# Kernel tuning notes

Measured on AMD Instinct MI355X. Metric: run time of the kernel, lower is better.

## Reference

```python
import jax, jax.numpy as jnp
import numpy as np

SIGMA = 4.0
KSIZE = 2 * int(4.0 * SIGMA + 0.5) + 1  # 33, anomalib AnomalyMapGenerator default


def _gauss_kernel():
    x = jnp.arange(KSIZE, dtype=jnp.float32) - (KSIZE - 1) / 2.0
    g = jnp.exp(-0.5 * (x / SIGMA) ** 2)
    return g / g.sum()


def _blur(img):
    # img: (B,1,H,W); separable Gaussian with reflect padding (kornia border_type='reflect')
    k = _gauss_kernel()
    p = (KSIZE - 1) // 2
    dn = ('NCHW', 'OIHW', 'NCHW')
    x = jnp.pad(img, ((0, 0), (0, 0), (p, p), (0, 0)), mode='reflect')
    x = jax.lax.conv_general_dilated(x, k.reshape(1, 1, KSIZE, 1), (1, 1), 'VALID', dimension_numbers=dn)
    x = jnp.pad(x, ((0, 0), (0, 0), (0, 0), (p, p)), mode='reflect')
    return jax.lax.conv_general_dilated(x, k.reshape(1, 1, 1, KSIZE), (1, 1), 'VALID', dimension_numbers=dn)


def _edist(x, y):
    # ||x-y||_2 via expanded quadratic, clamped at 0 (matches torch euclidean_dist)
    x2 = jnp.sum(x * x, axis=-1, keepdims=True)
    y2 = jnp.sum(y * y, axis=-1, keepdims=True)
    d2 = x2 - 2.0 * (x @ y.T) + y2.T
    return jnp.sqrt(jnp.clip(d2, 0.0))


def setup_inputs() -> dict:
    key = jax.random.key(0)
    k1, k2 = jax.random.split(key)
    return {
        'embedding': jax.random.normal(k1, (6272, 128), dtype=jnp.float32),
        'memory_bank': jax.random.normal(k2, (32768, 128), dtype=jnp.float32),
        'batch_size': 8,
        'width': 28,
        'height': 28,
        'out_size': 224,
        'num_neighbors': 9,
    }


def reference(embedding, memory_bank, batch_size, width, height, out_size, num_neighbors):
    N, D = embedding.shape
    M = memory_bank.shape[0]
    # --- nearest_neighbors(embedding, n_neighbors=1), euclidean metric ---
    dist = _edist(embedding, memory_bank)            # (N, M) dominant intermediate
    patch_scores = jnp.min(dist, axis=1)             # (N,)
    locations = jnp.argmin(dist, axis=1)             # (N,)
    P = N // batch_size
    patch_scores = patch_scores.reshape(batch_size, P)
    locations = locations.reshape(batch_size, P)
    # --- compute_anomaly_score (num_neighbors > 1 branch) ---
    b_idx = jnp.arange(batch_size)
    max_p = jnp.argmax(patch_scores, axis=1)                         # (B,)
    max_feat = embedding.reshape(batch_size, P, D)[b_idx, max_p]     # (B, D)
    score = patch_scores[b_idx, max_p]                               # (B,)
    nn_idx = locations[b_idx, max_p]                                 # (B,)
    nn_sample = memory_bank[nn_idx]                                  # (B, D)
    k = min(int(num_neighbors), M)
    d_nn = _edist(nn_sample, memory_bank)                            # (B, M)
    _, support = jax.lax.top_k(-d_nn, k)                             # (B, k) smallest distances
    mem_s = memory_bank[support]                                     # (B, k, D)
    qm = jnp.einsum('bd,bkd->bk', max_feat, mem_s)
    d2 = jnp.sum(max_feat * max_feat, -1, keepdims=True) - 2.0 * qm + jnp.sum(mem_s * mem_s, -1)
    dists = jnp.sqrt(jnp.clip(d2, 0.0))                              # (B, k)
    weights = (1.0 - jax.nn.softmax(dists, axis=1))[:, 0]
    pred_score = weights * score                                     # (B,)
    # --- anomaly map: bilinear upsample (align_corners=False) + Gaussian blur ---
    pm = patch_scores.reshape(batch_size, 1, width, height)
    amap = jax.image.resize(pm, (batch_size, 1, out_size, out_size), method='bilinear')
    anomaly_map = _blur(amap)
    return pred_score, anomaly_map
```

## Files before the change

### kernel.cpp

```cpp
#include <hip/hip_runtime.h>
#include <hip/hip_bf16.h>

#define N_EMB   6272
#define M_BANK  32768
#define D_DIM   128
#define KPA     128
#define KPB     128
#define BATCH   8
#define P_PATCH 784
#define GRID_WH 28
#define OUT_WH  224
#define KNN     9
#define KSIZE   33
#define KRAD    16

typedef unsigned long long ull;
typedef short bf16x8 __attribute__((ext_vector_type(8)));
typedef float f32x4  __attribute__((ext_vector_type(4)));

#define WS_MINPACK 0
#define WS_X2      50176
#define WS_Y2      75264
#define WS_BSCORE  231424
#define WS_BMAXP   231456
#define WS_BNN     231488
#define WS_DNN     231552
#define WS_APK     2885888
#define WS_BPK     7702784
#define WS_CAND    32868608

__device__ __forceinline__ ull umin64(ull a, ull b) { return a < b ? a : b; }
__device__ __forceinline__ ull umax64(ull a, ull b) { return a > b ? a : b; }

__device__ __forceinline__ void gload_lds16(const void* g, void* l) {
    __builtin_amdgcn_global_load_lds(
        (const __attribute__((address_space(1))) void*)g,
        (__attribute__((address_space(3))) void*)l, 16, 0, 0);
}

__global__ __launch_bounds__(256) void prep_kernel(
    const float* __restrict__ emb, const float* __restrict__ bank,
    unsigned short* __restrict__ Apk, unsigned short* __restrict__ Bpk,
    float* __restrict__ x2, float* __restrict__ y2, ull* __restrict__ minpack)
{
    const int tid = threadIdx.x;
    int gi = blockIdx.x * 256 + tid;
    if (gi < N_EMB) minpack[gi] = ~0ull;

    const int w    = blockIdx.x * 4 + (tid >> 6);
    const int lane = tid & 63;

    const float* src;
    unsigned short* dst;
    float* sq;
    if (w < N_EMB) {
        src = emb + (size_t)w * D_DIM;
        dst = Apk + (size_t)w * KPA;
        sq  = x2 + w;
    } else {
        int m = w - N_EMB;
        src = bank + (size_t)m * D_DIM;
        dst = Bpk + (size_t)m * KPB;
        sq  = y2 + m;
    }
    float2 v = *(const float2*)&src[2 * lane];
    __hip_bfloat16 h0 = __float2bfloat16(v.x);
    __hip_bfloat16 h1 = __float2bfloat16(v.y);
    unsigned hb0 = *(unsigned short*)&h0, hb1 = *(unsigned short*)&h1;
    *(unsigned*)&dst[2 * lane] = hb0 | (hb1 << 16);

    float s = fmaf(v.x, v.x, v.y * v.y);
    #pragma unroll
    for (int off = 32; off > 0; off >>= 1) s += __shfl_down(s, off, 64);
    if (lane == 0) *sq = s;
}

__global__ __launch_bounds__(256, 4) void mfma_min_kernel(
    const unsigned short* __restrict__ Apk, const unsigned short* __restrict__ Bpk,
    const float* __restrict__ y2, ull* __restrict__ minpack)
{
    __shared__ __align__(16) unsigned short smem[4 * 128 * 32];
    const int PAN = 128 * 32;

    const int tid  = threadIdx.x;
    const int lane = tid & 63;
    const int wave = tid >> 6;
    const int wr = wave >> 1, wc = wave & 1;
    const int n0 = blockIdx.y * 128;
    const int m0 = blockIdx.x * 128;

    const int srow = tid >> 2;
    const int sseg = tid & 3;
    const int ssw  = sseg ^ ((srow >> 1) & 3);

    const int qa = lane >> 4;
    const int ra = lane & 15;
    const int qsw = qa ^ ((ra >> 1) & 3);

    f32x4 acc[4][4];
    #pragma unroll
    for (int i = 0; i < 4; ++i)
        #pragma unroll
        for (int j = 0; j < 4; ++j)
            acc[i][j] = (f32x4){0.f, 0.f, 0.f, 0.f};

    const unsigned short* gA = Apk + (size_t)(n0 + srow) * KPA + ssw * 8;
    const unsigned short* gB = Bpk + (size_t)(m0 + srow) * KPB + ssw * 8;
    const int lof0 = srow * 32 + sseg * 8;
    const int lof1 = (srow + 64) * 32 + sseg * 8;

    gload_lds16(gA,            &smem[lof0]);
    gload_lds16(gA + 64 * KPA, &smem[lof1]);
    gload_lds16(gB,            &smem[2 * PAN + lof0]);
    gload_lds16(gB + 64 * KPB, &smem[2 * PAN + lof1]);

    #define STEP(s, VM) { \
         \
        asm volatile("s_barrier" ::: "memory"); \
        if ((s) < 3) { \
            const int ko = ((s) + 1) * 32; \
            const int nb = ((s) + 1) & 1; \
            gload_lds16(gA + ko,            &smem[nb * PAN + lof0]); \
            gload_lds16(gA + ko + 64 * KPA, &smem[nb * PAN + lof1]); \
            gload_lds16(gB + ko,            &smem[(2 + nb) * PAN + lof0]); \
            gload_lds16(gB + ko + 64 * KPB, &smem[(2 + nb) * PAN + lof1]); \
        } \
         \
        asm volatile("s_waitcnt vmcnt(" #VM ")" ::: "memory"); \
         \
        asm volatile("s_barrier" ::: "memory"); \
        const unsigned short* As = &smem[((s) & 1) * PAN]; \
        const unsigned short* Bs = &smem[(2 + ((s) & 1)) * PAN]; \
        bf16x8 bfr[4]; \
        _Pragma("unroll") \
        for (int j = 0; j < 4; ++j) \
            bfr[j] = *(const bf16x8*)&Bs[(wc * 64 + j * 16 + ra) * 32 + qsw * 8]; \
        { \
            bf16x8 af0 = *(const bf16x8*)&As[(wr * 64 +  0 + ra) * 32 + qsw * 8]; \
            bf16x8 af1 = *(const bf16x8*)&As[(wr * 64 + 16 + ra) * 32 + qsw * 8]; \
            _Pragma("unroll") \
            for (int j = 0; j < 4; ++j) \
                acc[0][j] = __builtin_amdgcn_mfma_f32_16x16x32_bf16(af0, bfr[j], acc[0][j], 0, 0, 0); \
            _Pragma("unroll") \
            for (int j = 0; j < 4; ++j) \
                acc[1][j] = __builtin_amdgcn_mfma_f32_16x16x32_bf16(af1, bfr[j], acc[1][j], 0, 0, 0); \
            __builtin_amdgcn_sched_barrier(0); \
            bf16x8 af2 = *(const bf16x8*)&As[(wr * 64 + 32 + ra) * 32 + qsw * 8]; \
            bf16x8 af3 = *(const bf16x8*)&As[(wr * 64 + 48 + ra) * 32 + qsw * 8]; \
            _Pragma("unroll") \
            for (int j = 0; j < 4; ++j) \
                acc[2][j] = __builtin_amdgcn_mfma_f32_16x16x32_bf16(af2, bfr[j], acc[2][j], 0, 0, 0); \
            _Pragma("unroll") \
            for (int j = 0; j < 4; ++j) \
                acc[3][j] = __builtin_amdgcn_mfma_f32_16x16x32_bf16(af3, bfr[j], acc[3][j], 0, 0, 0); \
        } \
    }

    STEP(0, 4) STEP(1, 4) STEP(2, 4) STEP(3, 0)
    #undef STEP

    float y2k[4];
    unsigned mj[4];
    #pragma unroll
    for (int j = 0; j < 4; ++j) {
        const int m = m0 + wc * 64 + j * 16 + ra;
        y2k[j] = y2[m] + 1000.0f;
        mj[j]  = (unsigned)m;
    }

    ull (*red2)[32] = (ull (*)[32])smem;

    __syncthreads();

    #pragma unroll
    for (int i = 0; i < 4; ++i) {
        #pragma unroll
        for (int r = 0; r < 4; ++r) {
            const int rowl = wr * 64 + i * 16 + qa * 4 + r;
            ull mn = ~0ull;
            #pragma unroll
            for (int j = 0; j < 4; ++j) {
                float key = fmaf(-2.0f, acc[i][j][r], y2k[j]);
                ull p = ((ull)__float_as_uint(key) << 32) | mj[j];
                mn = umin64(mn, p);
            }
            red2[rowl][wc * 16 + ra] = mn;
        }
    }
    __syncthreads();
    if (tid < 128) {
        const int l = tid & 63;
        ull mn = ~0ull;
        #pragma unroll
        for (int k = 0; k < 32; ++k)
            mn = umin64(mn, red2[tid][(k + l) & 31]);
        atomicMin(&minpack[n0 + tid], mn);
    }
}

__device__ __forceinline__ int refl224(int i) {
    if (i < 0) i = -i;
    if (i >= OUT_WH) i = 2 * (OUT_WH - 1) - i;
    return i;
}

__global__ __launch_bounds__(256) void blur_argmax_kernel(
    const ull* __restrict__ minpack, const float* __restrict__ x2,
    float* __restrict__ bscore, int* __restrict__ bmaxp, int* __restrict__ bnn,
    float* __restrict__ outp)
{
    __shared__ float g[KSIZE];
    __shared__ float ps[P_PATCH];
    __shared__ float q[GRID_WH * OUT_WH];
    __shared__ float hq[GRID_WH * OUT_WH];
    __shared__ float wrow[32][GRID_WH];
    __shared__ ull red[256];

    const int tid = threadIdx.x;
    const int band = blockIdx.x;
    const int b    = blockIdx.y;

    if (tid < KSIZE) {
        float x = (tid - KRAD) * 0.25f;
        g[tid] = __expf(-0.5f * x * x);
    }
    ull local = 0;
    for (int i = tid; i < P_PATCH; i += 256) {
        ull mp = minpack[b * P_PATCH + i];
        float key = __uint_as_float((unsigned)(mp >> 32));
        float d2 = key - 1000.0f + x2[b * P_PATCH + i];
        float sc = sqrtf(fmaxf(d2, 0.0f));
        ps[i] = sc;
        ull pk = ((ull)__float_as_uint(sc) << 32) | (unsigned)(i ^ 0xFFFFFFFFu);
        local = umax64(local, pk);
    }
    red[tid] = local;
    __syncthreads();
    if (tid == 0) {
        float s = 0.0f;
        for (int i = 0; i < KSIZE; ++i) s += g[i];
        float inv = 1.0f / s;
        for (int i = 0; i < KSIZE; ++i) g[i] *= inv;
    }
    for (int s = 128; s > 0; s >>= 1) {
        if (tid < s) red[tid] = umax64(red[tid], red[tid + s]);
        __syncthreads();
    }
    if (band == 0 && tid == 0) {
        ull r = red[0];
        int p = (int)(((unsigned)(r & 0xFFFFFFFFu)) ^ 0xFFFFFFFFu);
        bscore[b] = __uint_as_float((unsigned)(r >> 32));
        bmaxp[b]  = p;
        bnn[b]    = (int)(minpack[b * P_PATCH + p] & 0xFFFFFFFFu);
    }

    for (int i = tid; i < GRID_WH * OUT_WH; i += 256) {
        int gy = i / OUT_WH, x = i - gy * OUT_WH;
        float cx = (2 * x - 7) * 0.0625f;
        int ix = (int)floorf(cx); float fx = cx - ix;
        int x0 = min(max(ix, 0), GRID_WH - 1), x1 = min(max(ix + 1, 0), GRID_WH - 1);
        q[i] = ps[gy * GRID_WH + x0] * (1.0f - fx) + ps[gy * GRID_WH + x1] * fx;
    }

    if (tid < 32) {
        int y = band * 32 + tid;
        for (int gy = 0; gy < GRID_WH; ++gy) wrow[tid][gy] = 0.0f;
        for (int t = 0; t < KSIZE; ++t) {
            int yy = refl224(y - KRAD + t);
            float cy = (2 * yy - 7) * 0.0625f;
            int iy = (int)floorf(cy); float fy = cy - iy;
            int y0 = min(max(iy, 0), GRID_WH - 1), y1 = min(max(iy + 1, 0), GRID_WH - 1);
            wrow[tid][y0] += g[t] * (1.0f - fy);
            wrow[tid][y1] += g[t] * fy;
        }
    }
    __syncthreads();

    for (int i = tid; i < GRID_WH * OUT_WH; i += 256) {
        int gy = i / OUT_WH, x = i - gy * OUT_WH;
        float s = 0.0f;
        #pragma unroll
        for (int t = 0; t < KSIZE; ++t)
            s = fmaf(g[t], q[gy * OUT_WH + refl224(x - KRAD + t)], s);
        hq[i] = s;
    }
    __syncthreads();

    const int yl = tid >> 3;
    const int xbase = (tid & 7) * 28;
    const int y = band * 32 + yl;
    float* orow = outp + ((size_t)b * OUT_WH + y) * OUT_WH;
    for (int i = 0; i < 28; ++i) {
        int x = xbase + i;
        float s = 0.0f;
        #pragma unroll
        for (int gy = 0; gy < GRID_WH; ++gy)
            s = fmaf(wrow[yl][gy], hq[gy * OUT_WH + x], s);
        orow[x] = s;
    }
}

__global__ __launch_bounds__(256) void dnn_kernel(
    const float* __restrict__ bank, const float* __restrict__ y2,
    const int* __restrict__ bnn, float* __restrict__ dnn)
{
    __shared__ float nn[BATCH][D_DIM];
    __shared__ float nny2[BATCH];
    int tid = threadIdx.x;
    for (int i = tid; i < BATCH * D_DIM; i += 256) {
        int b = i >> 7, d = i & 127;
        nn[b][d] = bank[(size_t)bnn[b] * D_DIM + d];
    }
    if (tid < BATCH) nny2[tid] = y2[bnn[tid]];
    __syncthreads();

    int w = tid >> 6, lane = tid & 63;
    int m = blockIdx.x * 4 + w;
    float2 v = *(const float2*)&bank[(size_t)m * D_DIM + 2 * lane];
    float part[BATCH];
    #pragma unroll
    for (int b = 0; b < BATCH; ++b)
        part[b] = fmaf(v.x, nn[b][2 * lane], v.y * nn[b][2 * lane + 1]);
    #pragma unroll
    for (int b = 0; b < BATCH; ++b) {
        float s = part[b];
        #pragma unroll
        for (int off = 32; off > 0; off >>= 1) s += __shfl_down(s, off, 64);
        if (lane == 0) {
            float d2 = nny2[b] + y2[m] - 2.0f * s;
            dnn[b * M_BANK + m] = sqrtf(fmaxf(d2, 0.0f));
        }
    }
}

__global__ __launch_bounds__(256) void topk_part_kernel(
    const float* __restrict__ dnn, ull* __restrict__ cand)
{
    __shared__ ull vals[1024];
    __shared__ ull red[256];
    const int tid = threadIdx.x;
    const int b = blockIdx.y, ch = blockIdx.x;
    const int base = ch * 1024;

    #pragma unroll
    for (int j = 0; j < 4; ++j) {
        int i = base + tid + j * 256;
        vals[tid + j * 256] = ((ull)__float_as_uint(dnn[b * M_BANK + i]) << 32) | (unsigned)i;
    }
    __syncthreads();

    for (int k = 0; k < KNN; ++k) {
        ull local = vals[tid];
        #pragma unroll
        for (int j = 1; j < 4; ++j) local = umin64(local, vals[tid + j * 256]);
        red[tid] = local;
        __syncthreads();
        for (int s = 128; s > 0; s >>= 1) {
            if (tid < s) red[tid] = umin64(red[tid], red[tid + s]);
            __syncthreads();
        }
        ull win = red[0];
        if (tid == 0) cand[(b * 32 + ch) * KNN + k] = win;
        #pragma unroll
        for (int j = 0; j < 4; ++j)
            if (vals[tid + j * 256] == win) vals[tid + j * 256] = ~0ull;
        __syncthreads();
    }
}

__global__ __launch_bounds__(256) void topk_final_kernel(
    const ull* __restrict__ cand,
    const float* __restrict__ emb, const float* __restrict__ bank,
    const float* __restrict__ x2, const float* __restrict__ y2,
    const float* __restrict__ bscore, const int* __restrict__ bmaxp,
    float* __restrict__ out)
{
    __shared__ ull vals[512];
    __shared__ ull red[256];
    __shared__ int chosen[KNN];
    __shared__ float dists[KNN];
    const int tid = threadIdx.x;
    const int b = blockIdx.x;

    vals[tid]       = (tid < 32 * KNN) ? cand[b * 32 * KNN + tid] : ~0ull;
    vals[tid + 256] = (tid + 256 < 32 * KNN) ? cand[b * 32 * KNN + tid + 256] : ~0ull;
    __syncthreads();

    for (int k = 0; k < KNN; ++k) {
        red[tid] = umin64(vals[tid], vals[tid + 256]);
        __syncthreads();
        for (int s = 128; s > 0; s >>= 1) {
            if (tid < s) red[tid] = umin64(red[tid], red[tid + s]);
            __syncthreads();
        }
        ull win = red[0];
        if (tid == 0) chosen[k] = (int)(win & 0xFFFFFFFFu);
        if (vals[tid] == win) vals[tid] = ~0ull;
        if (vals[tid + 256] == win) vals[tid + 256] = ~0ull;
        __syncthreads();
    }

    const int e = b * P_PATCH + bmaxp[b];
    if (tid < KNN) {
        const float* mf = emb + (size_t)e * D_DIM;
        const float* ms = bank + (size_t)chosen[tid] * D_DIM;
        float dot = 0.0f;
        for (int d = 0; d < D_DIM; ++d) dot = fmaf(mf[d], ms[d], dot);
        float d2 = x2[e] - 2.0f * dot + y2[chosen[tid]];
        dists[tid] = sqrtf(fmaxf(d2, 0.0f));
    }
    __syncthreads();
    if (tid == 0) {
        float mx = dists[0];
        for (int k = 1; k < KNN; ++k) mx = fmaxf(mx, dists[k]);
        float s = 0.0f;
        for (int k = 0; k < KNN; ++k) s += expf(dists[k] - mx);
        float w = 1.0f - expf(dists[0] - mx) / s;
        out[b] = w * bscore[b];
    }
}

extern "C" void kernel_launch(void* const* d_in, const int* in_sizes, int n_in,
                              void* d_out, int out_size, void* d_ws, size_t ws_size,
                              hipStream_t stream) {
    const float* emb  = (const float*)d_in[0];
    const float* bank = (const float*)d_in[1];
    float* out = (float*)d_out;

    char* ws = (char*)d_ws;
    ull*   minpack = (ull*)(ws + WS_MINPACK);
    float* x2      = (float*)(ws + WS_X2);
    float* y2      = (float*)(ws + WS_Y2);
    float* bscore  = (float*)(ws + WS_BSCORE);
    int*   bmaxp   = (int*)(ws + WS_BMAXP);
    int*   bnn     = (int*)(ws + WS_BNN);
    float* dnn     = (float*)(ws + WS_DNN);
    unsigned short* Apk = (unsigned short*)(ws + WS_APK);
    unsigned short* Bpk = (unsigned short*)(ws + WS_BPK);
    ull*   cand    = (ull*)(ws + WS_CAND);

    prep_kernel<<<(N_EMB + M_BANK) / 4, 256, 0, stream>>>(emb, bank, Apk, Bpk, x2, y2, minpack);
    {
        dim3 grid(M_BANK / 128, N_EMB / 128);
        mfma_min_kernel<<<grid, 256, 0, stream>>>(Apk, Bpk, y2, minpack);
    }
    {
        dim3 grid(OUT_WH / 32, BATCH);
        blur_argmax_kernel<<<grid, 256, 0, stream>>>(minpack, x2, bscore, bmaxp, bnn, out + BATCH);
    }
    dnn_kernel<<<M_BANK / 4, 256, 0, stream>>>(bank, y2, bnn, dnn);
    {
        dim3 grid(32, BATCH);
        topk_part_kernel<<<grid, 256, 0, stream>>>(dnn, cand);
    }
    topk_final_kernel<<<BATCH, 256, 0, stream>>>(cand, emb, bank, x2, y2, bscore, bmaxp, out);
}
```

Before: 226.3 us.

## Fuse top-k final stage into partial kernel via last-block counter; cheaper min epilogue

Removes the separate topk_final kernel launch. The last block to finish topk_part, detected with a global atomic counter and threadfence, now does the final 9-way selection and the softmax weight using wave-level shuffle reductions instead of shared-memory tree reductions. The MFMA epilogue also replaces the 64-bit packed min over four columns with float fminf plus index selects, packing to 64 bits only once. This saves one launch and some ALU work, but adds a serialized tail in a single block and a global counter that must be reset after every call.

```diff
diff --git a/kernel.cpp b/kernel.cpp
--- a/kernel.cpp
+++ b/kernel.cpp
@@ -37,6 +37,8 @@
         (const __attribute__((address_space(1))) void*)g,
         (__attribute__((address_space(3))) void*)l, 16, 0, 0);
 }
+
+__device__ unsigned tpf_ctr = 0;
 
 __global__ __launch_bounds__(256) void prep_kernel(
     const float* __restrict__ emb, const float* __restrict__ bank,
@@ -177,14 +179,14 @@
         #pragma unroll
         for (int r = 0; r < 4; ++r) {
             const int rowl = wr * 64 + i * 16 + qa * 4 + r;
-            ull mn = ~0ull;
-            #pragma unroll
-            for (int j = 0; j < 4; ++j) {
-                float key = fmaf(-2.0f, acc[i][j][r], y2k[j]);
-                ull p = ((ull)__float_as_uint(key) << 32) | mj[j];
-                mn = umin64(mn, p);
-            }
-            red2[rowl][wc * 16 + ra] = mn;
+            float k0 = fmaf(-2.0f, acc[i][0][r], y2k[0]);
+            float k1 = fmaf(-2.0f, acc[i][1][r], y2k[1]);
+            float k2 = fmaf(-2.0f, acc[i][2][r], y2k[2]);
+            float k3 = fmaf(-2.0f, acc[i][3][r], y2k[3]);
+            float m01 = fminf(k0, k1); unsigned i01 = (k1 < k0) ? mj[1] : mj[0];
+            float m23 = fminf(k2, k3); unsigned i23 = (k3 < k2) ? mj[3] : mj[2];
+            float mm  = fminf(m01, m23); unsigned ii = (m23 < m01) ? i23 : i01;
+            red2[rowl][wc * 16 + ra] = ((ull)__float_as_uint(mm) << 32) | ii;
         }
     }
     __syncthreads();
@@ -334,10 +336,15 @@
 }
 
 __global__ __launch_bounds__(256) void topk_part_kernel(
-    const float* __restrict__ dnn, ull* __restrict__ cand)
+    const float* __restrict__ dnn, ull* __restrict__ cand,
+    const float* __restrict__ emb, const float* __restrict__ bank,
+    const float* __restrict__ x2, const float* __restrict__ y2,
+    const float* __restrict__ bscore, const int* __restrict__ bmaxp,
+    float* __restrict__ out)
 {
     __shared__ ull vals[1024];
     __shared__ ull red[256];
+    __shared__ unsigned lastflag;
     const int tid = threadIdx.x;
     const int b = blockIdx.y, ch = blockIdx.x;
     const int base = ch * 1024;
@@ -366,58 +373,63 @@
             if (vals[tid + j * 256] == win) vals[tid + j * 256] = ~0ull;
         __syncthreads();
     }
-}
-
-__global__ __launch_bounds__(256) void topk_final_kernel(
-    const ull* __restrict__ cand,
-    const float* __restrict__ emb, const float* __restrict__ bank,
-    const float* __restrict__ x2, const float* __restrict__ y2,
-    const float* __restrict__ bscore, const int* __restrict__ bmaxp,
-    float* __restrict__ out)
-{
-    __shared__ ull vals[512];
-    __shared__ ull red[256];
-    __shared__ int chosen[KNN];
-    __shared__ float dists[KNN];
-    const int tid = threadIdx.x;
-    const int b = blockIdx.x;
-
-    vals[tid]       = (tid < 32 * KNN) ? cand[b * 32 * KNN + tid] : ~0ull;
-    vals[tid + 256] = (tid + 256 < 32 * KNN) ? cand[b * 32 * KNN + tid + 256] : ~0ull;
-    __syncthreads();
-
-    for (int k = 0; k < KNN; ++k) {
-        red[tid] = umin64(vals[tid], vals[tid + 256]);
-        __syncthreads();
-        for (int s = 128; s > 0; s >>= 1) {
-            if (tid < s) red[tid] = umin64(red[tid], red[tid + s]);
-            __syncthreads();
-        }
-        ull win = red[0];
-        if (tid == 0) chosen[k] = (int)(win & 0xFFFFFFFFu);
-        if (vals[tid] == win) vals[tid] = ~0ull;
-        if (vals[tid + 256] == win) vals[tid + 256] = ~0ull;
-        __syncthreads();
-    }
-
-    const int e = b * P_PATCH + bmaxp[b];
-    if (tid < KNN) {
-        const float* mf = emb + (size_t)e * D_DIM;
-        const float* ms = bank + (size_t)chosen[tid] * D_DIM;
-        float dot = 0.0f;
-        for (int d = 0; d < D_DIM; ++d) dot = fmaf(mf[d], ms[d], dot);
-        float d2 = x2[e] - 2.0f * dot + y2[chosen[tid]];
-        dists[tid] = sqrtf(fmaxf(d2, 0.0f));
-    }
-    __syncthreads();
+
     if (tid == 0) {
-        float mx = dists[0];
-        for (int k = 1; k < KNN; ++k) mx = fmaxf(mx, dists[k]);
-        float s = 0.0f;
-        for (int k = 0; k < KNN; ++k) s += expf(dists[k] - mx);
-        float w = 1.0f - expf(dists[0] - mx) / s;
-        out[b] = w * bscore[b];
-    }
+        __threadfence();
+        unsigned t = atomicAdd(&tpf_ctr, 1u);
+        lastflag = (t == 8u * 32u - 1u);
+    }
+    __syncthreads();
+    if (!lastflag) return;
+    __threadfence();
+
+    const int wv = tid >> 6, ln = tid & 63;
+    #pragma unroll
+    for (int half = 0; half < 2; ++half) {
+        const int bb = wv + half * 4;
+        const ull* cb = cand + (size_t)bb * 32 * KNN;
+        ull c0 = cb[ln];
+        ull c1 = cb[ln + 64];
+        ull c2 = cb[ln + 128];
+        ull c3 = cb[ln + 192];
+        ull c4 = (ln < 32) ? cb[ln + 256] : ~0ull;
+        const int e = bb * P_PATCH + bmaxp[bb];
+        const float mf0 = emb[(size_t)e * D_DIM + 2 * ln];
+        const float mf1 = emb[(size_t)e * D_DIM + 2 * ln + 1];
+        const float xe = x2[e];
+        float dists[KNN];
+        #pragma unroll
+        for (int k = 0; k < KNN; ++k) {
+            ull mn = umin64(umin64(umin64(c0, c1), umin64(c2, c3)), c4);
+            #pragma unroll
+            for (int s = 1; s < 64; s <<= 1)
+                mn = umin64(mn, (ull)__shfl_xor((unsigned long long)mn, s, 64));
+            if (c0 == mn) c0 = ~0ull;
+            if (c1 == mn) c1 = ~0ull;
+            if (c2 == mn) c2 = ~0ull;
+            if (c3 == mn) c3 = ~0ull;
+            if (c4 == mn) c4 = ~0ull;
+            const int m = (int)(mn & 0xFFFFFFFFu);
+            float dot = fmaf(mf0, bank[(size_t)m * D_DIM + 2 * ln],
+                             mf1 * bank[(size_t)m * D_DIM + 2 * ln + 1]);
+            #pragma unroll
+            for (int s = 1; s < 64; s <<= 1)
+                dot += __shfl_xor(dot, s, 64);
+            float d2 = xe - 2.0f * dot + y2[m];
+            dists[k] = sqrtf(fmaxf(d2, 0.0f));
+        }
+        if (ln == 0) {
+            float mx = dists[0];
+            #pragma unroll
+            for (int k = 1; k < KNN; ++k) mx = fmaxf(mx, dists[k]);
+            float ssum = 0.0f;
+            #pragma unroll
+            for (int k = 0; k < KNN; ++k) ssum += expf(dists[k] - mx);
+            float wgt = 1.0f - expf(dists[0] - mx) / ssum;
+            out[bb] = wgt * bscore[bb];
+        }
+    }
+    if (tid == 0) atomicExch(&tpf_ctr, 0u);
 }
 
 extern "C" void kernel_launch(void* const* d_in, const int* in_sizes, int n_in,
@@ -451,7 +463,6 @@
     dnn_kernel<<<M_BANK / 4, 256, 0, stream>>>(bank, y2, bnn, dnn);
     {
         dim3 grid(32, BATCH);
-        topk_part_kernel<<<grid, 256, 0, stream>>>(dnn, cand);
-    }
-    topk_final_kernel<<<BATCH, 256, 0, stream>>>(cand, emb, bank, x2, y2, bscore, bmaxp, out);
-}
+        topk_part_kernel<<<grid, 256, 0, stream>>>(dnn, cand, emb, bank, x2, y2, bscore, bmaxp, out);
+    }
+}
```

Result: slower. 235.3 us (+3.9%).
